# Performance work log

Measured on AMD Instinct MI355X. Metric: run time of the kernel, lower is better.

The kernel has to match this reference:

```python
import jax, jax.numpy as jnp
import numpy as np

B, C, H, W = 4, 256, 128, 128
D = 256            # attention hidden_dim (== C, so no output_proj)
HID = 1024         # mlp hidden = int(C * 4.0)
EPS = 1e-5


def setup_inputs() -> dict:
    key = jax.random.key(0)
    ks = jax.random.split(key, 16)
    s = 0.02
    return {
        "x": jax.random.normal(ks[0], (B, C, H, W), jnp.float32),
        "wq": jax.random.normal(ks[1], (C, D), jnp.float32) * s,
        "bq": jnp.zeros((D,), jnp.float32),
        "wk": jax.random.normal(ks[2], (C, D), jnp.float32) * s,
        "bk": jnp.zeros((D,), jnp.float32),
        "wv": jax.random.normal(ks[3], (C, D), jnp.float32) * s,
        "bv": jnp.zeros((D,), jnp.float32),
        "ln1_g": jnp.ones((C,), jnp.float32),
        "ln1_b": jnp.zeros((C,), jnp.float32),
        "ln2_g": jnp.ones((C,), jnp.float32),
        "ln2_b": jnp.zeros((C,), jnp.float32),
        "fc1_w": jax.random.normal(ks[4], (C, HID), jnp.float32) * s,
        "fc1_b": jnp.zeros((HID,), jnp.float32),
        "fc2_w": jax.random.normal(ks[5], (HID, C), jnp.float32) * s,
        "fc2_b": jnp.zeros((C,), jnp.float32),
    }


def _layernorm(x, g, b):
    m = jnp.mean(x, axis=-1, keepdims=True)
    v = jnp.mean(jnp.square(x - m), axis=-1, keepdims=True)
    return (x - m) * jax.lax.rsqrt(v + EPS) * g + b


def _neighborhoods(t):
    # t: [B,H,W,D] -> [B,H,W,9,D] 3x3 neighborhoods, zero-padded at borders
    tp = jnp.pad(t, ((0, 0), (1, 1), (1, 1), (0, 0)))
    h, w = t.shape[1], t.shape[2]
    return jnp.stack(
        [tp[:, dy:dy + h, dx:dx + w, :] for dy in range(3) for dx in range(3)],
        axis=3,
    )


def _valid_mask(h, w):
    # [H,W,9] bool: which of the 9 neighbors are inside the grid
    ys = jnp.arange(h)[:, None] * jnp.ones((1, w), jnp.int32)
    xs = jnp.arange(w)[None, :] * jnp.ones((h, 1), jnp.int32)
    top, bot = ys > 0, ys < h - 1
    lef, rig = xs > 0, xs < w - 1
    ones = jnp.ones((h, w), bool)
    return jnp.stack(
        [top & lef, top, top & rig, lef, ones, rig, bot & lef, bot, bot & rig],
        axis=-1,
    )


def reference(x, wq, bq, wk, bk, wv, bv, ln1_g, ln1_b, ln2_g, ln2_b,
              fc1_w, fc1_b, fc2_w, fc2_b):
    b_, c_, h_, w_ = x.shape
    xc = jnp.transpose(x, (0, 2, 3, 1))                    # [B,H,W,C]
    n1 = _layernorm(xc, ln1_g, ln1_b)
    q = n1 @ wq + bq                                       # [B,H,W,D]
    k = n1 @ wk + bk
    v = n1 @ wv + bv
    kn = _neighborhoods(k)                                  # [B,H,W,9,D]
    vn = _neighborhoods(v)
    scores = jnp.einsum('bhwd,bhwnd->bhwn', q, kn) / jnp.sqrt(jnp.float32(q.shape[-1]))
    mask = _valid_mask(h_, w_)                               # [H,W,9]
    scores = jnp.where(mask, scores, jnp.float32(-1e9))
    weights = jax.nn.softmax(scores, axis=-1)
    attn = jnp.einsum('bhwn,bhwnd->bhwd', weights, vn)       # [B,H,W,D]
    x1 = xc + attn                                           # residual 1
    n2 = _layernorm(x1, ln2_g, ln2_b)
    mlp = jax.nn.gelu(n2 @ fc1_w + fc1_b, approximate=False) @ fc2_w + fc2_b
    out = x1 + mlp
    return jnp.transpose(out, (0, 3, 1, 2))                  # [B,C,H,W]
```

## Files before the change

kernel.cpp:

```cpp
#include <hip/hip_runtime.h>
#include <hip/hip_bf16.h>
#include <math.h>

#define NPIX  65536
#define CCH   256
#define HWSZ  16384
#define WIDTH 128
#define HID   1024

typedef unsigned short u16;
typedef __bf16 bf16x8 __attribute__((ext_vector_type(8)));
typedef float  floatx4 __attribute__((ext_vector_type(4)));

__device__ __forceinline__ float bf2f(u16 u) {
  union { unsigned int i; float f; } c; c.i = ((unsigned int)u) << 16; return c.f;
}
__device__ __forceinline__ float bflo(unsigned int u) {
  union { unsigned int i; float f; } c; c.i = u << 16; return c.f;
}
__device__ __forceinline__ float bfhi(unsigned int u) {
  union { unsigned int i; float f; } c; c.i = u & 0xffff0000u; return c.f;
}
__device__ __forceinline__ u16 f2bf(float f) {
  union { float f; unsigned int i; } c; c.f = f;
  unsigned int x = c.i;
  x += 0x7fffu + ((x >> 16) & 1u);
  return (u16)(x >> 16);
}

__device__ __forceinline__ void async16(const void* g, void* l) {
  __builtin_amdgcn_global_load_lds(
      (const __attribute__((address_space(1))) void*)g,
      (__attribute__((address_space(3))) void*)l, 16, 0, 0);
}

__global__ __launch_bounds__(256) void wtrans_kernel(
    const float* __restrict__ src, u16* __restrict__ dst, int R, int C) {
  __shared__ float tile[32][33];
  const int tx = threadIdx.x & 31, ty = threadIdx.x >> 5;
  const int r0 = blockIdx.y * 32, c0 = blockIdx.x * 32;
#pragma unroll
  for (int i = 0; i < 32; i += 8)
    tile[ty + i][tx] = src[(size_t)(r0 + ty + i) * C + c0 + tx];
  __syncthreads();
#pragma unroll
  for (int i = 0; i < 32; i += 8)
    dst[(size_t)(c0 + ty + i) * R + r0 + tx] = f2bf(tile[tx][ty + i]);
}

__global__ __launch_bounds__(256) void concat_bias_kernel(
    const float* __restrict__ bq, const float* __restrict__ bk,
    const float* __restrict__ bv, float* __restrict__ dst) {
  const int i = blockIdx.x * 256 + threadIdx.x;
  if (i < 256) dst[i] = bq[i];
  else if (i < 512) dst[i] = bk[i - 256];
  else if (i < 768) dst[i] = bv[i - 512];
}

__global__ __launch_bounds__(256) void ln1_kernel(
    const float* __restrict__ x, const float* __restrict__ g,
    const float* __restrict__ bb, u16* __restrict__ n1) {
  __shared__ float sx[32][257];
  __shared__ float sred[16][32];
  __shared__ float sm[32], sr[32];
  const int tx = threadIdx.x;
  const int p0 = blockIdx.x * 32;
  {
    const int pix = tx & 31, cpart = tx >> 5;
    const int p = p0 + pix;
    const int b = p >> 14, hw = p & (HWSZ - 1);
    const float* xb = x + ((size_t)b * CCH) * HWSZ + hw;
    float s = 0.f, s2 = 0.f;
#pragma unroll 4
    for (int i = 0; i < 32; i++) {
      const int c = cpart * 32 + i;
      const float v = xb[(size_t)c * HWSZ];
      sx[pix][c] = v;
      s += v; s2 += v * v;
    }
    sred[cpart][pix] = s; sred[8 + cpart][pix] = s2;
  }
  __syncthreads();
  if (tx < 32) {
    float s = 0.f, s2 = 0.f;
#pragma unroll
    for (int j = 0; j < 8; j++) { s += sred[j][tx]; s2 += sred[8 + j][tx]; }
    const float m = s * (1.0f / 256.0f);
    const float var = s2 * (1.0f / 256.0f) - m * m;
    sm[tx] = m; sr[tx] = rsqrtf(var + 1e-5f);
  }
  __syncthreads();
  const float gc = g[tx], bc = bb[tx];
#pragma unroll 4
  for (int i = 0; i < 32; i++) {
    const float v = (sx[i][tx] - sm[i]) * sr[i] * gc + bc;
    n1[(size_t)(p0 + i) * CCH + tx] = f2bf(v);
  }
}

__global__ __launch_bounds__(256) void res_ln2_kernel(
    const float* __restrict__ x, const u16* __restrict__ attn,
    const float* __restrict__ g, const float* __restrict__ bb,
    float* __restrict__ x1, u16* __restrict__ n2) {
  __shared__ float sx[32][257];
  __shared__ float sred[16][32];
  __shared__ float sm[32], sr[32];
  const int tx = threadIdx.x;
  const int p0 = blockIdx.x * 32;
  {
    const int pix = tx & 31, cpart = tx >> 5;
    const int p = p0 + pix;
    const int b = p >> 14, hw = p & (HWSZ - 1);
    const float* xb = x + ((size_t)b * CCH) * HWSZ + hw;
#pragma unroll 4
    for (int i = 0; i < 32; i++) {
      const int c = cpart * 32 + i;
      sx[pix][c] = xb[(size_t)c * HWSZ];
    }
  }
  __syncthreads();
#pragma unroll 4
  for (int i = 0; i < 32; i++) {
    const float v = sx[i][tx] + bf2f(attn[(size_t)(p0 + i) * CCH + tx]);
    sx[i][tx] = v;
    x1[(size_t)(p0 + i) * CCH + tx] = v;
  }
  __syncthreads();
  {
    const int pix = tx & 31, cpart = tx >> 5;
    float s = 0.f, s2 = 0.f;
#pragma unroll 4
    for (int i = 0; i < 32; i++) {
      const float v = sx[pix][cpart * 32 + i];
      s += v; s2 += v * v;
    }
    sred[cpart][pix] = s; sred[8 + cpart][pix] = s2;
  }
  __syncthreads();
  if (tx < 32) {
    float s = 0.f, s2 = 0.f;
#pragma unroll
    for (int j = 0; j < 8; j++) { s += sred[j][tx]; s2 += sred[8 + j][tx]; }
    const float m = s * (1.0f / 256.0f);
    const float var = s2 * (1.0f / 256.0f) - m * m;
    sm[tx] = m; sr[tx] = rsqrtf(var + 1e-5f);
  }
  __syncthreads();
  const float gc = g[tx], bc = bb[tx];
#pragma unroll 4
  for (int i = 0; i < 32; i++) {
    const float v = (sx[i][tx] - sm[i]) * sr[i] * gc + bc;
    n2[(size_t)(p0 + i) * CCH + tx] = f2bf(v);
  }
}

__global__ __launch_bounds__(256) void attn_kernel(
    const u16* __restrict__ qkv, u16* __restrict__ attn) {
  const int tid = threadIdx.x;
  const int wave = tid >> 6, lane = tid & 63;
  const int p = blockIdx.x * 4 + wave;
  const int hw = p & (HWSZ - 1);
  const int hh = hw >> 7, ww = hw & (WIDTH - 1);
  const u16* rowp = qkv + (size_t)p * 768 + lane * 4;
  const uint2 qr = *(const uint2*)rowp;
  const float qf0 = bflo(qr.x), qf1 = bfhi(qr.x);
  const float qf2 = bflo(qr.y), qf3 = bfhi(qr.y);
  float sc[9];
#pragma unroll
  for (int n = 0; n < 9; n++) {
    const int dy = n / 3 - 1, dx = n % 3 - 1;
    const int y = hh + dy, x2 = ww + dx;
    float s = -1e30f;
    if (y >= 0 && y < 128 && x2 >= 0 && x2 < 128) {
      const uint2 kr = *(const uint2*)(rowp + 256 + (dy * WIDTH + dx) * 768);
      float d = qf0 * bflo(kr.x) + qf1 * bfhi(kr.x)
              + qf2 * bflo(kr.y) + qf3 * bfhi(kr.y);
#pragma unroll
      for (int o = 32; o >= 1; o >>= 1) d += __shfl_xor(d, o, 64);
      s = d * 0.0625f;
    }
    sc[n] = s;
  }
  float mx = sc[0];
#pragma unroll
  for (int n = 1; n < 9; n++) mx = fmaxf(mx, sc[n]);
  float wgt[9], wsum = 0.f;
#pragma unroll
  for (int n = 0; n < 9; n++) { wgt[n] = __expf(sc[n] - mx); wsum += wgt[n]; }
  const float inv = 1.0f / wsum;
  float a0 = 0.f, a1 = 0.f, a2 = 0.f, a3 = 0.f;
#pragma unroll
  for (int n = 0; n < 9; n++) {
    const int dy = n / 3 - 1, dx = n % 3 - 1;
    const int y = hh + dy, x2 = ww + dx;
    if (y >= 0 && y < 128 && x2 >= 0 && x2 < 128) {
      const uint2 vr = *(const uint2*)(rowp + 512 + (dy * WIDTH + dx) * 768);
      const float wn = wgt[n] * inv;
      a0 += wn * bflo(vr.x); a1 += wn * bfhi(vr.x);
      a2 += wn * bflo(vr.y); a3 += wn * bfhi(vr.y);
    }
  }
  uint2 o;
  o.x = ((unsigned int)f2bf(a1) << 16) | (unsigned int)f2bf(a0);
  o.y = ((unsigned int)f2bf(a3) << 16) | (unsigned int)f2bf(a2);
  *(uint2*)(attn + (size_t)p * CCH + lane * 4) = o;
}

template <int NCH, int KCH, int KT, int EPI>
__global__ __launch_bounds__(256, 2) void gemm_regA(
    const u16* __restrict__ A, const u16* __restrict__ BT,
    const float* __restrict__ bias, const float* __restrict__ x1,
    u16* __restrict__ outb, float* __restrict__ outf, int Kglb) {
  constexpr int KS   = KT / 32;
  constexpr int K16  = KT / 8;
  constexpr int CPC  = 512 / KT;
  constexpr int CSU  = KT;
  constexpr int GSU  = (8 * KT * 2 + 64) / 2;
  constexpr int NACC = (KCH > 1) ? NCH : 1;
  __shared__ u16 sB[8 * GSU];

  const int tid  = threadIdx.x;
  const int wave = tid >> 6, lane = tid & 63;
  const int quad = lane >> 4, l16 = lane & 15;
  const int m0 = blockIdx.x * 128;
  const int wr  = (wave & 1) * 64;
  const int wcq = (wave >> 1) * 32;

  const int c0 = wcq + l16, c1 = c0 + 16;
  const int sb0 = (c0 >> 3) * GSU + (c0 & 7) * CSU;
  const int sb1 = (c1 >> 3) * GSU + (c1 & 7) * CSU;

  const int stc   = wave * 16;
  const int stcol = (lane * 16) / (KT * 2);
  const int stk   = lane & (K16 - 1);

  const u16* aRow = A + (size_t)(m0 + wr + l16) * Kglb + quad * 8;

  bf16x8 afr[4][KS];
  floatx4 acc[NACC][4][2];

  auto stage = [&](int idx) {
    const int kc = idx / NCH, ch = idx % NCH;
    const u16* gB = BT + kc * KT + stk * 8;
#pragma unroll
    for (int i = 0; i < 16 / CPC; i++) {
      const int cc = stc + i * CPC;
      async16(gB + (size_t)(ch * 64 + cc + stcol) * Kglb,
              sB + (cc >> 3) * GSU + (cc & 7) * CSU);
    }
  };
  auto loadA = [&](int kc) {
#pragma unroll
    for (int mi = 0; mi < 4; mi++)
#pragma unroll
      for (int ks = 0; ks < KS; ks++)
        afr[mi][ks] = *(const bf16x8*)(aRow + (size_t)mi * 16 * Kglb + kc * KT + ks * 32);
  };
  auto compute = [&](int ci) {
#pragma unroll
    for (int ks = 0; ks < KS; ks++) {
      const int ko = (ks * 4 + quad) * 8;
      const bf16x8 b0 = *(const bf16x8*)&sB[sb0 + ko];
      const bf16x8 b1 = *(const bf16x8*)&sB[sb1 + ko];
#pragma unroll
      for (int mi = 0; mi < 4; mi++) {
        acc[ci][mi][0] = __builtin_amdgcn_mfma_f32_16x16x32_bf16(
            afr[mi][ks], b0, acc[ci][mi][0], 0, 0, 0);
        acc[ci][mi][1] = __builtin_amdgcn_mfma_f32_16x16x32_bf16(
            afr[mi][ks], b1, acc[ci][mi][1], 0, 0, 0);
      }
    }
  };
  auto epilogue = [&](int ci, int ch) {
#pragma unroll
    for (int mi = 0; mi < 4; mi++)
#pragma unroll
      for (int ni = 0; ni < 2; ni++) {
        const int col = ch * 64 + wcq + ni * 16 + l16;
        const float bs = bias[col];
#pragma unroll
        for (int r = 0; r < 4; r++) {
          const int row = m0 + wr + mi * 16 + quad * 4 + r;
          float val = acc[ci][mi][ni][r] + bs;
          if constexpr (EPI == 0) {
            outb[(size_t)row * 768 + col] = f2bf(val);
          } else if constexpr (EPI == 1) {
            const float t = 0.7978845608028654f * (val + 0.044715f * val * val * val);
            const float e = __expf(2.0f * t);
            const float th = 1.0f - 2.0f / (e + 1.0f);
            val = 0.5f * val * (1.0f + th);
            outb[(size_t)row * HID + col] = f2bf(val);
          } else {
            val += x1[(size_t)row * CCH + col];
            outf[((size_t)((row >> 14) * CCH + col)) * HWSZ + (row & (HWSZ - 1))] = val;
          }
        }
      }
  };

  if constexpr (KCH == 1) {
    stage(0);
    loadA(0);
#pragma unroll 1
    for (int ch = 0; ch < NCH; ++ch) {
      __syncthreads();
#pragma unroll
      for (int mi = 0; mi < 4; mi++)
#pragma unroll
        for (int ni = 0; ni < 2; ni++)
          acc[0][mi][ni] = (floatx4){0.f, 0.f, 0.f, 0.f};
      compute(0);
      __syncthreads();
      if (ch + 1 < NCH) stage(ch + 1);
      epilogue(0, ch);
    }
  } else {
    stage(0);
#pragma unroll
    for (int ci = 0; ci < NACC; ci++)
#pragma unroll
      for (int mi = 0; mi < 4; mi++)
#pragma unroll
        for (int ni = 0; ni < 2; ni++)
          acc[ci][mi][ni] = (floatx4){0.f, 0.f, 0.f, 0.f};
#pragma unroll 1
    for (int kc = 0; kc < KCH; ++kc) {
      loadA(kc);
#pragma unroll
      for (int ch = 0; ch < NCH; ++ch) {
        __syncthreads();
        compute(ch);
        __syncthreads();
        const int nxt = kc * NCH + ch + 1;
        if (nxt < KCH * NCH) stage(nxt);
      }
    }
#pragma unroll
    for (int ch = 0; ch < NCH; ++ch) epilogue(ch, ch);
  }
}

extern "C" void kernel_launch(void* const* d_in, const int* in_sizes, int n_in,
                              void* d_out, int out_size, void* d_ws, size_t ws_size,
                              hipStream_t stream) {
  const float* x    = (const float*)d_in[0];
  const float* wq   = (const float*)d_in[1];
  const float* bq   = (const float*)d_in[2];
  const float* wk   = (const float*)d_in[3];
  const float* bk   = (const float*)d_in[4];
  const float* wv   = (const float*)d_in[5];
  const float* bv   = (const float*)d_in[6];
  const float* ln1g = (const float*)d_in[7];
  const float* ln1b = (const float*)d_in[8];
  const float* ln2g = (const float*)d_in[9];
  const float* ln2b = (const float*)d_in[10];
  const float* fc1w = (const float*)d_in[11];
  const float* fc1b = (const float*)d_in[12];
  const float* fc2w = (const float*)d_in[13];
  const float* fc2b = (const float*)d_in[14];
  float* out = (float*)d_out;

  char* ws = (char*)d_ws;
  const size_t MB = (size_t)1 << 20;
  float* x1   = (float*)(ws);
  u16* qkv    = (u16*)(ws + 64 * MB);
  u16* hbuf   = (u16*)(ws + 64 * MB);
  u16* n1     = (u16*)(ws + 160 * MB);
  u16* attnb  = n1;
  u16* n2     = (u16*)(ws + 192 * MB);
  u16* wqkvT  = (u16*)(ws + 224 * MB);
  u16* f1T    = wqkvT + 768 * 256;
  u16* f2T    = f1T + 1024 * 256;
  float* bqkv = (float*)(f2T + 256 * 1024);

  dim3 blk(256);
  wtrans_kernel<<<dim3(8, 8), blk, 0, stream>>>(wq, wqkvT, 256, 256);
  wtrans_kernel<<<dim3(8, 8), blk, 0, stream>>>(wk, wqkvT + 256 * 256, 256, 256);
  wtrans_kernel<<<dim3(8, 8), blk, 0, stream>>>(wv, wqkvT + 512 * 256, 256, 256);
  wtrans_kernel<<<dim3(32, 8), blk, 0, stream>>>(fc1w, f1T, 256, 1024);
  wtrans_kernel<<<dim3(8, 32), blk, 0, stream>>>(fc2w, f2T, 1024, 256);
  concat_bias_kernel<<<dim3(3), blk, 0, stream>>>(bq, bk, bv, bqkv);

  ln1_kernel<<<NPIX / 32, blk, 0, stream>>>(x, ln1g, ln1b, n1);

  gemm_regA<12, 1, 256, 0><<<dim3(512), blk, 0, stream>>>(
      n1, wqkvT, bqkv, nullptr, qkv, nullptr, 256);

  attn_kernel<<<NPIX / 4, blk, 0, stream>>>(qkv, attnb);

  res_ln2_kernel<<<NPIX / 32, blk, 0, stream>>>(x, attnb, ln2g, ln2b, x1, n2);

  gemm_regA<16, 1, 256, 1><<<dim3(512), blk, 0, stream>>>(
      n2, f1T, fc1b, nullptr, hbuf, nullptr, 256);

  gemm_regA<4, 8, 128, 2><<<dim3(512), blk, 0, stream>>>(
      hbuf, f2T, fc2b, x1, nullptr, out, 1024);
}
```

Baseline: 485.8 us.

## Halve GEMM row tile, swizzle B LDS layout, vectorize fc2 epilogue stores

The GEMM row tile per block drops from 128 to 64, doubling the grid to 1024 blocks and raising launch bounds to 4 blocks per CU to improve occupancy and latency hiding. The B staging layout in LDS becomes a k-major, column-interleaved arrangement so fragment reads are contiguous and free of bank conflicts without padding. The fc2 epilogue now writes four consecutive rows as one float4 store into the NCHW output. The trade-off is that each B tile is reused across half as many rows, so B traffic from global memory and LDS doubles.

```diff
diff --git a/kernel.cpp b/kernel.cpp
--- a/kernel.cpp
+++ b/kernel.cpp
@@ -207,63 +207,63 @@
 }
 
 template <int NCH, int KCH, int KT, int EPI>
-__global__ __launch_bounds__(256, 2) void gemm_regA(
+__global__ __launch_bounds__(256, 4) void gemm_regA(
     const u16* __restrict__ A, const u16* __restrict__ BT,
     const float* __restrict__ bias, const float* __restrict__ x1,
     u16* __restrict__ outb, float* __restrict__ outf, int Kglb) {
-  constexpr int KS   = KT / 32;
-  constexpr int K16  = KT / 8;
-  constexpr int CPC  = 512 / KT;
-  constexpr int CSU  = KT;
-  constexpr int GSU  = (8 * KT * 2 + 64) / 2;
-  constexpr int NACC = (KCH > 1) ? NCH : 1;
-  __shared__ u16 sB[8 * GSU];
+  constexpr int KS    = KT / 32;
+  constexpr int K16   = KT / 8;
+  constexpr int SLOT  = 64 * K16;
+  constexpr int CALLS = SLOT / 256;
+  constexpr int COLPC = 256 / K16;
+  constexpr int NACC  = (KCH > 1) ? NCH : 1;
+  __shared__ u16 sB[SLOT * 8];
 
   const int tid  = threadIdx.x;
   const int wave = tid >> 6, lane = tid & 63;
   const int quad = lane >> 4, l16 = lane & 15;
-  const int m0 = blockIdx.x * 128;
-  const int wr  = (wave & 1) * 64;
+  const int m0  = blockIdx.x * 64;
+  const int wr  = (wave & 1) * 32;
   const int wcq = (wave >> 1) * 32;
 
-  const int c0 = wcq + l16, c1 = c0 + 16;
-  const int sb0 = (c0 >> 3) * GSU + (c0 & 7) * CSU;
-  const int sb1 = (c1 >> 3) * GSU + (c1 & 7) * CSU;
-
-  const int stc   = wave * 16;
-  const int stcol = (lane * 16) / (KT * 2);
-  const int stk   = lane & (K16 - 1);
+  const int stCol = (tid & 7) + ((K16 == 16) ? ((tid >> 7) << 3) : 0);
+  const int stU   = (K16 == 16) ? ((tid & 127) >> 3) : (tid >> 3);
+  const u16* stBase = BT + (size_t)stCol * Kglb + stU * 8;
+  u16* stLds = sB + wave * 512;
+
+  int sbN[2];
+#pragma unroll
+  for (int ni = 0; ni < 2; ni++) {
+    const int c = wcq + ni * 16 + l16;
+    sbN[ni] = ((c >> 3) * (8 * K16) + (c & 7)) * 8 + quad * 64;
+  }
 
   const u16* aRow = A + (size_t)(m0 + wr + l16) * Kglb + quad * 8;
 
-  bf16x8 afr[4][KS];
-  floatx4 acc[NACC][4][2];
+  bf16x8 afr[2][KS];
+  floatx4 acc[NACC][2][2];
 
   auto stage = [&](int idx) {
     const int kc = idx / NCH, ch = idx % NCH;
-    const u16* gB = BT + kc * KT + stk * 8;
-#pragma unroll
-    for (int i = 0; i < 16 / CPC; i++) {
-      const int cc = stc + i * CPC;
-      async16(gB + (size_t)(ch * 64 + cc + stcol) * Kglb,
-              sB + (cc >> 3) * GSU + (cc & 7) * CSU);
-    }
+    const u16* g = stBase + (size_t)(ch * 64) * Kglb + kc * KT;
+#pragma unroll
+    for (int i = 0; i < CALLS; i++)
+      async16(g + (size_t)(i * COLPC) * Kglb, stLds + i * 2048);
   };
   auto loadA = [&](int kc) {
 #pragma unroll
-    for (int mi = 0; mi < 4; mi++)
+    for (int mi = 0; mi < 2; mi++)
 #pragma unroll
       for (int ks = 0; ks < KS; ks++)
         afr[mi][ks] = *(const bf16x8*)(aRow + (size_t)mi * 16 * Kglb + kc * KT + ks * 32);
   };
-  auto compute = [&](int ci) {
+  auto computeC = [&](int ci) {
 #pragma unroll
     for (int ks = 0; ks < KS; ks++) {
-      const int ko = (ks * 4 + quad) * 8;
-      const bf16x8 b0 = *(const bf16x8*)&sB[sb0 + ko];
-      const bf16x8 b1 = *(const bf16x8*)&sB[sb1 + ko];
-#pragma unroll
-      for (int mi = 0; mi < 4; mi++) {
+      const bf16x8 b0 = *(const bf16x8*)&sB[sbN[0] + ks * 256];
+      const bf16x8 b1 = *(const bf16x8*)&sB[sbN[1] + ks * 256];
+#pragma unroll
+      for (int mi = 0; mi < 2; mi++) {
         acc[ci][mi][0] = __builtin_amdgcn_mfma_f32_16x16x32_bf16(
             afr[mi][ks], b0, acc[ci][mi][0], 0, 0, 0);
         acc[ci][mi][1] = __builtin_amdgcn_mfma_f32_16x16x32_bf16(
@@ -273,26 +273,31 @@
   };
   auto epilogue = [&](int ci, int ch) {
 #pragma unroll
-    for (int mi = 0; mi < 4; mi++)
+    for (int mi = 0; mi < 2; mi++)
 #pragma unroll
       for (int ni = 0; ni < 2; ni++) {
         const int col = ch * 64 + wcq + ni * 16 + l16;
         const float bs = bias[col];
-#pragma unroll
-        for (int r = 0; r < 4; r++) {
-          const int row = m0 + wr + mi * 16 + quad * 4 + r;
-          float val = acc[ci][mi][ni][r] + bs;
-          if constexpr (EPI == 0) {
-            outb[(size_t)row * 768 + col] = f2bf(val);
-          } else if constexpr (EPI == 1) {
-            const float t = 0.7978845608028654f * (val + 0.044715f * val * val * val);
-            const float e = __expf(2.0f * t);
-            const float th = 1.0f - 2.0f / (e + 1.0f);
-            val = 0.5f * val * (1.0f + th);
-            outb[(size_t)row * HID + col] = f2bf(val);
-          } else {
-            val += x1[(size_t)row * CCH + col];
-            outf[((size_t)((row >> 14) * CCH + col)) * HWSZ + (row & (HWSZ - 1))] = val;
+        const int row0 = m0 + wr + mi * 16 + quad * 4;
+        if constexpr (EPI == 2) {
+          floatx4 vv;
+#pragma unroll
+          for (int r = 0; r < 4; r++)
+            vv[r] = acc[ci][mi][ni][r] + bs + x1[(size_t)(row0 + r) * CCH + col];
+          *(floatx4*)&outf[((size_t)((row0 >> 14) * CCH + col)) * HWSZ + (row0 & (HWSZ - 1))] = vv;
+        } else {
+#pragma unroll
+          for (int r = 0; r < 4; r++) {
+            float val = acc[ci][mi][ni][r] + bs;
+            if constexpr (EPI == 0) {
+              outb[(size_t)(row0 + r) * 768 + col] = f2bf(val);
+            } else {
+              const float t = 0.7978845608028654f * (val + 0.044715f * val * val * val);
+              const float e = __expf(2.0f * t);
+              const float th = 1.0f - 2.0f / (e + 1.0f);
+              val = 0.5f * val * (1.0f + th);
+              outb[(size_t)(row0 + r) * HID + col] = f2bf(val);
+            }
           }
         }
       }
@@ -305,11 +310,11 @@
     for (int ch = 0; ch < NCH; ++ch) {
       __syncthreads();
 #pragma unroll
-      for (int mi = 0; mi < 4; mi++)
+      for (int mi = 0; mi < 2; mi++)
 #pragma unroll
         for (int ni = 0; ni < 2; ni++)
           acc[0][mi][ni] = (floatx4){0.f, 0.f, 0.f, 0.f};
-      compute(0);
+      computeC(0);
       __syncthreads();
       if (ch + 1 < NCH) stage(ch + 1);
       epilogue(0, ch);
@@ -319,7 +324,7 @@
 #pragma unroll
     for (int ci = 0; ci < NACC; ci++)
 #pragma unroll
-      for (int mi = 0; mi < 4; mi++)
+      for (int mi = 0; mi < 2; mi++)
 #pragma unroll
         for (int ni = 0; ni < 2; ni++)
           acc[ci][mi][ni] = (floatx4){0.f, 0.f, 0.f, 0.f};
@@ -329,7 +334,7 @@
 #pragma unroll
       for (int ch = 0; ch < NCH; ++ch) {
         __syncthreads();
-        compute(ch);
+        computeC(ch);
         __syncthreads();
         const int nxt = kc * NCH + ch + 1;
         if (nxt < KCH * NCH) stage(nxt);
@@ -383,16 +388,16 @@
 
   ln1_kernel<<<NPIX / 32, blk, 0, stream>>>(x, ln1g, ln1b, n1);
 
-  gemm_regA<12, 1, 256, 0><<<dim3(512), blk, 0, stream>>>(
+  gemm_regA<12, 1, 256, 0><<<dim3(NPIX / 64), blk, 0, stream>>>(
       n1, wqkvT, bqkv, nullptr, qkv, nullptr, 256);
 
   attn_kernel<<<NPIX / 4, blk, 0, stream>>>(qkv, attnb);
 
   res_ln2_kernel<<<NPIX / 32, blk, 0, stream>>>(x, attnb, ln2g, ln2b, x1, n2);
 
-  gemm_regA<16, 1, 256, 1><<<dim3(512), blk, 0, stream>>>(
+  gemm_regA<16, 1, 256, 1><<<dim3(NPIX / 64), blk, 0, stream>>>(
       n2, f1T, fc1b, nullptr, hbuf, nullptr, 256);
 
-  gemm_regA<4, 8, 128, 2><<<dim3(512), blk, 0, stream>>>(
+  gemm_regA<4, 8, 128, 2><<<dim3(NPIX / 64), blk, 0, stream>>>(
       hbuf, f2T, fc2b, x1, nullptr, out, 1024);
 }
```

After: 534.3 us. 1.1x slower.
